# Performance work log

Hardware: AMD Instinct MI355X
Metric: run time of the kernel (lower is better)

## Reference

```python
import jax, jax.numpy as jnp
import numpy as np

FFT_LEN = 512
HOP_LEN = 256
N_BLOCK = 4
N_BIN = FFT_LEN // 2 + 1  # 257
STATE_FACTOR = 0.99999
ALPHA_E = 0.7
BETA_F = 0.1
BATCH = 4096
N_MIC = 1


def setup_inputs() -> dict:
    key = jax.random.key(0)
    ks = jax.random.split(key, 7)
    return {
        "mic": jax.random.normal(ks[0], (BATCH, HOP_LEN, N_MIC), jnp.float32),
        "loudspeaker_buffer": jax.random.normal(ks[1], (BATCH, (N_BLOCK + 1) * HOP_LEN), jnp.float32),
        "phi_e": jax.random.uniform(ks[2], (BATCH, N_BIN, N_MIC), jnp.float32),
        "phi_f": jax.random.uniform(ks[3], (BATCH, N_BIN, N_BLOCK, N_MIC), jnp.float32),
        "P1": jax.random.uniform(ks[4], (BATCH, N_BIN, N_BLOCK, N_MIC), jnp.float32),
        "H_post_real": 0.1 * jax.random.normal(ks[5], (BATCH, N_BIN, N_BLOCK, N_MIC), jnp.float32),
        "H_post_imag": 0.1 * jax.random.normal(ks[6], (BATCH, N_BIN, N_BLOCK, N_MIC), jnp.float32),
    }


def reference(mic, loudspeaker_buffer, phi_e, phi_f, P1, H_post_real, H_post_imag):
    B = mic.shape[0]
    sf2 = STATE_FACTOR * STATE_FACTOR
    H_post = jax.lax.complex(H_post_real, H_post_imag)  # [B, n_bin, n_block, n_mic]

    # STFT of loudspeaker buffer: rectangular window, center=False -> n_block frames
    frame_idx = jnp.arange(N_BLOCK)[:, None] * HOP_LEN + jnp.arange(FFT_LEN)[None, :]
    frames = loudspeaker_buffer[:, frame_idx]              # [B, n_block, fft_len]
    X = jnp.swapaxes(jnp.fft.rfft(frames, axis=-1), 1, 2)  # [B, n_bin, n_block]

    # zero-padded rFFT of mic frame
    zpad = jnp.zeros((B, FFT_LEN - HOP_LEN, N_MIC), mic.dtype)
    fd_mic = jnp.fft.rfft(jnp.concatenate([zpad, mic], axis=1), n=FFT_LEN, axis=1)  # [B, n_bin, n_mic]

    H_prior = H_post
    # a-priori feedback estimate
    fd_fb_hat = jnp.sum(X[..., None] * H_prior, axis=2)                     # [B, n_bin, n_mic]
    est_fb = jnp.fft.irfft(fd_fb_hat, FFT_LEN, axis=1)[:, HOP_LEN:, :]      # [B, hop, n_mic]
    fd_est_fb = jnp.fft.rfft(jnp.concatenate([zpad, est_fb], axis=1), n=FFT_LEN, axis=1)
    E = fd_mic - fd_est_fb                                                  # [B, n_bin, n_mic]

    phi_e = ALPHA_E * phi_e + (1.0 - ALPHA_E) * jnp.abs(E) ** 2

    # Kalman gain
    phi_f = BETA_F * phi_f + (1.0 - BETA_F) * jnp.abs(H_prior) ** 2
    phi_n = (1.0 - sf2) * phi_f
    Xr = jnp.abs(X) ** 2                                                    # [B, n_bin, n_block]
    U = Xr[..., None] * P1                                                  # [B, n_bin, n_block, n_mic]
    R = U + 2.0 * phi_e[:, :, None, :] + 1e-10
    K = P1 * jnp.conj(X)[..., None] / R                                     # [B, n_bin, n_block, n_mic]
    P0 = jax.lax.stop_gradient(P1) - 0.5 * jax.lax.stop_gradient(jnp.abs(K) ** 2 * R)
    P1_new = sf2 * P0 + phi_n  # state update (not part of returned output)

    # filter update via gradient-constrained overlap-save
    dH = jnp.fft.irfft(K * E[:, :, None, :], FFT_LEN, axis=1)               # [B, fft_len, n_block, n_mic]
    mask = (jnp.arange(FFT_LEN) < HOP_LEN).astype(dH.dtype)[None, :, None, None]
    fd_dH = jnp.fft.rfft(dH * mask, n=FFT_LEN, axis=1)                      # [B, n_bin, n_block, n_mic]
    H_post_new = STATE_FACTOR * (H_prior + fd_dH)

    # a-posteriori feedback estimate and enhanced frame
    fd_fb_hat2 = jnp.sum(X[..., None] * H_post_new, axis=2)
    est_fb2 = jnp.fft.irfft(fd_fb_hat2, FFT_LEN, axis=1)[:, HOP_LEN:, :]
    enhanced = mic - est_fb2                                                # [B, hop, n_mic]
    return enhanced
```

## Files before the change

### kernel.cpp

```cpp
#include <hip/hip_runtime.h>
#include <math.h>

#define SF 0.99999f
#define PI2 6.283185307179586476925f
#define SWZ(c) ((c) ^ (((c) >> 4) & 15))
#define LDSFENCE() asm volatile("" ::: "memory")

template<int SGN>
__device__ __forceinline__ void twmul(float& ur, float& ui, float c, float s) {
    const float ss = (SGN < 0) ? -s : s;
    const float r = ur * c - ui * ss;
    const float i = ui * c + ur * ss;
    ur = r; ui = i;
}

template<int SGN>
__device__ __forceinline__ void bfly8(float* ur, float* ui) {
    const float C2 = 0.70710678118654752440f;
    float ar[4], ai[4], br[4], bi[4];
#pragma unroll
    for (int m = 0; m < 4; ++m) {
        ar[m] = ur[m] + ur[m + 4]; ai[m] = ui[m] + ui[m + 4];
        br[m] = ur[m] - ur[m + 4]; bi[m] = ui[m] - ui[m + 4];
    }
    float b1r, b1i, b2r, b2i, b3r, b3i;
    if (SGN < 0) {
        b1r = C2 * (br[1] + bi[1]); b1i = C2 * (bi[1] - br[1]);
        b2r = bi[2];                b2i = -br[2];
        b3r = C2 * (bi[3] - br[3]); b3i = -C2 * (br[3] + bi[3]);
    } else {
        b1r = C2 * (br[1] - bi[1]); b1i = C2 * (bi[1] + br[1]);
        b2r = -bi[2];               b2i = br[2];
        b3r = -C2 * (br[3] + bi[3]); b3i = C2 * (br[3] - bi[3]);
    }
    const float e0r = ar[0] + ar[2], e0i = ai[0] + ai[2];
    const float e1r = ar[0] - ar[2], e1i = ai[0] - ai[2];
    const float o0r = ar[1] + ar[3], o0i = ai[1] + ai[3];
    const float o1r = ar[1] - ar[3], o1i = ai[1] - ai[3];
    ur[0] = e0r + o0r; ui[0] = e0i + o0i;
    ur[4] = e0r - o0r; ui[4] = e0i - o0i;
    if (SGN < 0) { ur[2] = e1r + o1i; ui[2] = e1i - o1r; ur[6] = e1r - o1i; ui[6] = e1i + o1r; }
    else         { ur[2] = e1r - o1i; ui[2] = e1i + o1r; ur[6] = e1r + o1i; ui[6] = e1i - o1r; }
    const float f0r = br[0] + b2r, f0i = bi[0] + b2i;
    const float f1r = br[0] - b2r, f1i = bi[0] - b2i;
    const float g0r = b1r + b3r, g0i = b1i + b3i;
    const float g1r = b1r - b3r, g1i = b1i - b3i;
    ur[1] = f0r + g0r; ui[1] = f0i + g0i;
    ur[5] = f0r - g0r; ui[5] = f0i - g0i;
    if (SGN < 0) { ur[3] = f1r + g1i; ui[3] = f1i - g1r; ur[7] = f1r - g1i; ui[7] = f1i + g1r; }
    else         { ur[3] = f1r - g1i; ui[3] = f1i + g1r; ur[7] = f1r + g1i; ui[7] = f1i - g1r; }
}

template<int SGN>
__device__ __forceinline__ void fft512w(float* ur, float* ui,
                                        float2* __restrict__ buf,
                                        const float2* __restrict__ tw2,
                                        const float2* __restrict__ tw3,
                                        const int* ra, int t) {
    bfly8<SGN>(ur, ui);
    LDSFENCE();
#pragma unroll
    for (int m = 0; m < 8; ++m) buf[SWZ(8 * t + m)] = make_float2(ur[m], ui[m]);
    LDSFENCE();
#pragma unroll
    for (int m = 0; m < 8; ++m) { const float2 v = buf[ra[m]]; ur[m] = v.x; ui[m] = v.y; }
    const int k2 = t & 7;
#pragma unroll
    for (int m = 1; m < 8; ++m) { const float2 w = tw2[m * 8 + k2]; twmul<SGN>(ur[m], ui[m], w.x, w.y); }
    bfly8<SGN>(ur, ui);
    const int jj = ((t >> 3) << 6) + k2;
    LDSFENCE();
#pragma unroll
    for (int m = 0; m < 8; ++m) buf[SWZ(jj + 8 * m)] = make_float2(ur[m], ui[m]);
    LDSFENCE();
#pragma unroll
    for (int m = 0; m < 8; ++m) { const float2 v = buf[ra[m]]; ur[m] = v.x; ui[m] = v.y; }
#pragma unroll
    for (int m = 1; m < 8; ++m) { const float2 w = tw3[m * 64 + t]; twmul<SGN>(ur[m], ui[m], w.x, w.y); }
    bfly8<SGN>(ur, ui);
    LDSFENCE();
}

__global__ __launch_bounds__(256, 2) void pbfd_kernel(
    const float* __restrict__ g_mic,
    const float* __restrict__ g_lsb,
    const float* __restrict__ g_phie,
    const float* __restrict__ g_p1,
    const float* __restrict__ g_hr,
    const float* __restrict__ g_hi,
    float* __restrict__ g_out,
    int B) {
    __shared__ float2 tw2[64];
    __shared__ float2 tw3[512];
    __shared__ float2 xch[4][512];

    const int tid = threadIdx.x;
    for (int e = tid; e < 512; e += 256) {
        const int m = e >> 6, tt = e & 63;
        float s, c;
        sincosf(PI2 * (float)(m * tt) * (1.0f / 512.0f), &s, &c);
        tw3[e] = make_float2(c, s);
    }
    if (tid < 64) {
        const int m = tid >> 3, k = tid & 7;
        float s, c;
        sincosf(PI2 * (float)(m * k) * (1.0f / 64.0f), &s, &c);
        tw2[tid] = make_float2(c, s);
    }
    __syncthreads();

    const int w = tid >> 6;
    const int t = tid & 63;
    const int elem = blockIdx.x * 4 + w;
    if (elem >= B) return;
    float2* buf = &xch[w][0];
    const int ml = (64 - t) & 63;

    int ra[8];
#pragma unroll
    for (int m = 0; m < 8; ++m) ra[m] = SWZ(t + 64 * m);

    float mv[4];
    {
        const float* mp = g_mic + (size_t)elem * 256;
#pragma unroll
        for (int q = 0; q < 4; ++q) mv[q] = mp[t + 64 * q];
    }

    float xr[4][4], xi[4][4], xn[4];
    {
        const float* lb = g_lsb + (size_t)elem * 1280;
#pragma unroll
        for (int pr = 0; pr < 2; ++pr) {
            float ur[8], ui[8];
#pragma unroll
            for (int m = 0; m < 8; ++m) {
                ur[m] = lb[(2 * pr) * 256 + t + 64 * m];
                ui[m] = lb[(2 * pr + 1) * 256 + t + 64 * m];
            }
            fft512w<-1>(ur, ui, buf, tw2, tw3, ra, t);
#pragma unroll
            for (int m = 0; m < 4; ++m) {
                float zmr = __shfl(ur[7 - m], ml);
                float zmi = __shfl(ui[7 - m], ml);
                if (t == 0) {
                    zmr = (m == 0) ? ur[0] : ur[8 - m];
                    zmi = (m == 0) ? ui[0] : ui[8 - m];
                }
                xr[2 * pr][m]     = 0.5f * (ur[m] + zmr);
                xi[2 * pr][m]     = 0.5f * (ui[m] - zmi);
                xr[2 * pr + 1][m] = 0.5f * (ui[m] + zmi);
                xi[2 * pr + 1][m] = -0.5f * (ur[m] - zmr);
            }
            if (t == 0) { xn[2 * pr] = ur[4]; xn[2 * pr + 1] = ui[4]; }
        }
    }

    auto herm_ifft = [&](const float cr[4], const float ci[4], float cn, float o4[4]) {
        float ur[8], ui[8];
#pragma unroll
        for (int m = 0; m < 4; ++m) { ur[m] = cr[m]; ui[m] = ci[m]; }
#pragma unroll
        for (int m = 4; m < 8; ++m) {
            ur[m] = __shfl(cr[7 - m], ml);
            ui[m] = -__shfl(ci[7 - m], ml);
        }
        if (t == 0) {
            ur[5] = cr[3]; ui[5] = -ci[3];
            ur[6] = cr[2]; ui[6] = -ci[2];
            ur[7] = cr[1]; ui[7] = -ci[1];
            ur[4] = cn; ui[4] = 0.f;
        }
        fft512w<1>(ur, ui, buf, tw2, tw3, ra, t);
#pragma unroll
        for (int q = 0; q < 4; ++q) o4[q] = ur[4 + q] * (1.0f / 512.0f);
    };

    float d4[4];
    float pn[4], en = 0.f, pen = 0.f;
    {
        float hr_[4][4], hi_[4][4], hn[4];
        {
            const float4* hr4 = (const float4*)g_hr + (size_t)elem * 257;
            const float4* hi4 = (const float4*)g_hi + (size_t)elem * 257;
#pragma unroll
            for (int m = 0; m < 4; ++m) {
                const float4 a = hr4[t + 64 * m];
                hr_[0][m] = a.x; hr_[1][m] = a.y; hr_[2][m] = a.z; hr_[3][m] = a.w;
            }
#pragma unroll
            for (int m = 0; m < 4; ++m) {
                const float4 b = hi4[t + 64 * m];
                hi_[0][m] = b.x; hi_[1][m] = b.y; hi_[2][m] = b.z; hi_[3][m] = b.w;
            }
            if (t == 0) {
                const float4 a = hr4[256];
                const float4 p = ((const float4*)g_p1)[(size_t)elem * 257 + 256];
                hn[0] = a.x; hn[1] = a.y; hn[2] = a.z; hn[3] = a.w;
                pn[0] = p.x; pn[1] = p.y; pn[2] = p.z; pn[3] = p.w;
            }
        }
        float cr[4], ci[4], cn = 0.f;
#pragma unroll
        for (int m = 0; m < 4; ++m) {
            float sr = 0.f, si = 0.f;
#pragma unroll
            for (int j = 0; j < 4; ++j) {
                sr += xr[j][m] * hr_[j][m] - xi[j][m] * hi_[j][m];
                si += xr[j][m] * hi_[j][m] + xi[j][m] * hr_[j][m];
            }
            cr[m] = sr; ci[m] = si;
        }
        if (t == 0) {
#pragma unroll
            for (int j = 0; j < 4; ++j) cn += xn[j] * hn[j];
        }
        float o4[4];
        herm_ifft(cr, ci, cn, o4);
#pragma unroll
        for (int q = 0; q < 4; ++q) d4[q] = mv[q] - o4[q];
    }

    float er[4], ei[4];
    {
        float ur[8], ui[8];
#pragma unroll
        for (int m = 0; m < 4; ++m) { ur[m] = 0.f; ui[m] = 0.f; }
#pragma unroll
        for (int q = 0; q < 4; ++q) { ur[4 + q] = d4[q]; ui[4 + q] = 0.f; }
        fft512w<-1>(ur, ui, buf, tw2, tw3, ra, t);
#pragma unroll
        for (int m = 0; m < 4; ++m) { er[m] = ur[m]; ei[m] = ui[m]; }
        if (t == 0) en = ur[4];
    }

    float pe[4];
    {
        const float* php = g_phie + (size_t)elem * 257;
#pragma unroll
        for (int m = 0; m < 4; ++m)
            pe[m] = 0.7f * php[t + 64 * m] + 0.3f * (er[m] * er[m] + ei[m] * ei[m]);
        if (t == 0) pen = 0.7f * php[256] + 0.3f * en * en;
    }

    float Dr[4] = {0, 0, 0, 0}, Di[4] = {0, 0, 0, 0};
    float dn = 0.f;
    {
        const float4* p14 = (const float4*)g_p1 + (size_t)elem * 257;
#pragma unroll
        for (int pr = 0; pr < 2; ++pr) {
            const int j0 = 2 * pr, j1 = 2 * pr + 1;
            float ur[8], ui[8], gr[4], gi[4];
#pragma unroll
            for (int m = 0; m < 4; ++m) {
                const float4 p = p14[t + 64 * m];
                const float pa = pr ? p.z : p.x;
                const float pb = pr ? p.w : p.y;
                const float xxa = xr[j0][m] * xr[j0][m] + xi[j0][m] * xi[j0][m];
                const float Ra = xxa * pa + 2.f * pe[m] + 1e-10f;
                const float ia = 1.f / Ra;
                const float kra = pa * xr[j0][m] * ia, kia = -pa * xi[j0][m] * ia;
                const float a_r = kra * er[m] - kia * ei[m];
                const float a_i = kra * ei[m] + kia * er[m];
                const float xxb = xr[j1][m] * xr[j1][m] + xi[j1][m] * xi[j1][m];
                const float Rb = xxb * pb + 2.f * pe[m] + 1e-10f;
                const float ib = 1.f / Rb;
                const float krb = pb * xr[j1][m] * ib, kib = -pb * xi[j1][m] * ib;
                const float b_r = krb * er[m] - kib * ei[m];
                const float b_i = krb * ei[m] + kib * er[m];
                ur[m] = a_r - b_i;  ui[m] = a_i + b_r;
                gr[m] = a_r + b_i;  gi[m] = b_r - a_i;
            }
#pragma unroll
            for (int m = 4; m < 8; ++m) {
                ur[m] = __shfl(gr[7 - m], ml);
                ui[m] = __shfl(gi[7 - m], ml);
            }
            if (t == 0) {
                ur[5] = gr[3]; ui[5] = gi[3];
                ur[6] = gr[2]; ui[6] = gi[2];
                ur[7] = gr[1]; ui[7] = gi[1];
                const float Rn0 = xn[j0] * xn[j0] * pn[j0] + 2.f * pen + 1e-10f;
                const float Rn1 = xn[j1] * xn[j1] * pn[j1] + 2.f * pen + 1e-10f;
                ur[4] = pn[j0] * xn[j0] / Rn0 * en;
                ui[4] = pn[j1] * xn[j1] / Rn1 * en;
            }
            fft512w<1>(ur, ui, buf, tw2, tw3, ra, t);
#pragma unroll
            for (int m = 0; m < 4; ++m) { ur[m] *= (1.0f / 512.0f); ui[m] *= (1.0f / 512.0f); }
#pragma unroll
            for (int m = 4; m < 8; ++m) { ur[m] = 0.f; ui[m] = 0.f; }
            fft512w<-1>(ur, ui, buf, tw2, tw3, ra, t);
#pragma unroll
            for (int m = 0; m < 4; ++m) {
                float zmr = __shfl(ur[7 - m], ml);
                float zmi = __shfl(ui[7 - m], ml);
                if (t == 0) {
                    zmr = (m == 0) ? ur[0] : ur[8 - m];
                    zmi = (m == 0) ? ui[0] : ui[8 - m];
                }
                const float f0r = 0.5f * (ur[m] + zmr), f0i = 0.5f * (ui[m] - zmi);
                const float f1r = 0.5f * (ui[m] + zmi), f1i = -0.5f * (ur[m] - zmr);
                Dr[m] += xr[j0][m] * f0r - xi[j0][m] * f0i + xr[j1][m] * f1r - xi[j1][m] * f1i;
                Di[m] += xr[j0][m] * f0i + xi[j0][m] * f0r + xr[j1][m] * f1i + xi[j1][m] * f1r;
            }
            if (t == 0) dn += xn[j0] * ur[4] + xn[j1] * ui[4];
        }
    }

    {
        float o4[4];
        herm_ifft(Dr, Di, dn, o4);
        float* op = g_out + (size_t)elem * 256;
#pragma unroll
        for (int q = 0; q < 4; ++q)
            op[t + 64 * q] = mv[q] - SF * ((mv[q] - d4[q]) + o4[q]);
    }
}

extern "C" void kernel_launch(void* const* d_in, const int* in_sizes, int n_in,
                              void* d_out, int out_size, void* d_ws, size_t ws_size,
                              hipStream_t stream) {
    const float* mic  = (const float*)d_in[0];
    const float* lsb  = (const float*)d_in[1];
    const float* phie = (const float*)d_in[2];
    const float* p1   = (const float*)d_in[4];
    const float* hr   = (const float*)d_in[5];
    const float* hi   = (const float*)d_in[6];
    float* out = (float*)d_out;

    const int B = in_sizes[0] / 256;
    const int blocks = (B + 3) / 4;
    pbfd_kernel<<<blocks, 256, 0, stream>>>(mic, lsb, phie, p1, hr, hi, out, B);
}
```

Measured before the change: 36.76 us.

## Launch one 64-thread wavefront per batch element with per-wave twiddle setup

Changes the launch from 256-thread blocks holding four batch elements to single-wavefront blocks that each handle one element. The block-wide __syncthreads after twiddle setup goes away, leaving only a compiler memory fence. Each wave now builds its own twiddle tables, and the 512-entry table is generated by repeated complex multiplication from one sincos instead of one sincos per entry. This cuts per-block LDS and removes cross-wave synchronization, but it multiplies twiddle setup work per element. Recurrence rounding may also slightly change twiddle accuracy.

```diff
diff --git a/kernel.cpp b/kernel.cpp
--- a/kernel.cpp
+++ b/kernel.cpp
@@ -81,40 +81,40 @@
     LDSFENCE();
 }
 
-__global__ __launch_bounds__(256, 2) void pbfd_kernel(
+__global__ __launch_bounds__(64, 4) void pbfd_kernel(
     const float* __restrict__ g_mic,
     const float* __restrict__ g_lsb,
     const float* __restrict__ g_phie,
     const float* __restrict__ g_p1,
     const float* __restrict__ g_hr,
     const float* __restrict__ g_hi,
-    float* __restrict__ g_out,
-    int B) {
+    float* __restrict__ g_out)
+{
     __shared__ float2 tw2[64];
     __shared__ float2 tw3[512];
-    __shared__ float2 xch[4][512];
-
-    const int tid = threadIdx.x;
-    for (int e = tid; e < 512; e += 256) {
-        const int m = e >> 6, tt = e & 63;
-        float s, c;
-        sincosf(PI2 * (float)(m * tt) * (1.0f / 512.0f), &s, &c);
-        tw3[e] = make_float2(c, s);
-    }
-    if (tid < 64) {
-        const int m = tid >> 3, k = tid & 7;
-        float s, c;
-        sincosf(PI2 * (float)(m * k) * (1.0f / 64.0f), &s, &c);
-        tw2[tid] = make_float2(c, s);
-    }
-    __syncthreads();
-
-    const int w = tid >> 6;
-    const int t = tid & 63;
-    const int elem = blockIdx.x * 4 + w;
-    if (elem >= B) return;
-    float2* buf = &xch[w][0];
+    __shared__ float2 xch[512];
+
+    const int t = threadIdx.x;
+    const int elem = blockIdx.x;
+    float2* buf = &xch[0];
     const int ml = (64 - t) & 63;
+
+    {
+        float s3, c3;
+        sincosf(PI2 * (float)t * (1.0f / 512.0f), &s3, &c3);
+        float cr = 1.f, ci = 0.f;
+#pragma unroll
+        for (int m = 0; m < 8; ++m) {
+            tw3[m * 64 + t] = make_float2(cr, ci);
+            const float nr = cr * c3 - ci * s3;
+            ci = ci * c3 + cr * s3;
+            cr = nr;
+        }
+        float s2, c2;
+        sincosf(PI2 * (float)((t >> 3) * (t & 7)) * (1.0f / 64.0f), &s2, &c2);
+        tw2[t] = make_float2(c2, s2);
+    }
+    LDSFENCE();
 
     int ra[8];
 #pragma unroll
@@ -330,6 +330,5 @@
     float* out = (float*)d_out;
 
     const int B = in_sizes[0] / 256;
-    const int blocks = (B + 3) / 4;
-    pbfd_kernel<<<blocks, 256, 0, stream>>>(mic, lsb, phie, p1, hr, hi, out, B);
-}
+    pbfd_kernel<<<B, 64, 0, stream>>>(mic, lsb, phie, p1, hr, hi, out);
+}
```

Result: slower. 50.19 us (+36.5%).

## Split each batch element across two wavefronts, one per block pair

Applied to the files above, without the earlier changes.

Each batch element now gets a 128-thread block, and each of its two wavefronts handles one pair of blocks (FFT of two frames, the filter product and the Kalman gradient). Partial sums for the feedback estimate and the filter update are combined through shared memory with block barriers, and only wave 0 runs the final inverse FFT and store. This halves per-wave serial work and register pressure, giving more parallelism. The cost is extra LDS traffic and syncs, the same work done twice (mic load, error FFT, phi_e), and wave 1 sitting idle at the end.

```diff
diff --git a/kernel.cpp b/kernel.cpp
--- a/kernel.cpp
+++ b/kernel.cpp
@@ -81,21 +81,28 @@
     LDSFENCE();
 }
 
-__global__ __launch_bounds__(256, 2) void pbfd_kernel(
+__global__ __launch_bounds__(128, 2) void pbfd_kernel(
     const float* __restrict__ g_mic,
     const float* __restrict__ g_lsb,
     const float* __restrict__ g_phie,
     const float* __restrict__ g_p1,
     const float* __restrict__ g_hr,
     const float* __restrict__ g_hi,
-    float* __restrict__ g_out,
-    int B) {
+    float* __restrict__ g_out)
+{
     __shared__ float2 tw2[64];
     __shared__ float2 tw3[512];
-    __shared__ float2 xch[4][512];
+    __shared__ float2 xch[2][512];
 
     const int tid = threadIdx.x;
-    for (int e = tid; e < 512; e += 256) {
+    const int w = tid >> 6;
+    const int t = tid & 63;
+    const int elem = blockIdx.x;
+    float2* buf  = &xch[w][0];
+    float2* bufo = &xch[1 ^ w][0];
+    const int ml = (64 - t) & 63;
+
+    for (int e = tid; e < 512; e += 128) {
         const int m = e >> 6, tt = e & 63;
         float s, c;
         sincosf(PI2 * (float)(m * tt) * (1.0f / 512.0f), &s, &c);
@@ -109,13 +116,6 @@
     }
     __syncthreads();
 
-    const int w = tid >> 6;
-    const int t = tid & 63;
-    const int elem = blockIdx.x * 4 + w;
-    if (elem >= B) return;
-    float2* buf = &xch[w][0];
-    const int ml = (64 - t) & 63;
-
     int ra[8];
 #pragma unroll
     for (int m = 0; m < 8; ++m) ra[m] = SWZ(t + 64 * m);
@@ -127,33 +127,30 @@
         for (int q = 0; q < 4; ++q) mv[q] = mp[t + 64 * q];
     }
 
-    float xr[4][4], xi[4][4], xn[4];
+    float xrl[2][4], xil[2][4], xnl[2];
     {
         const float* lb = g_lsb + (size_t)elem * 1280;
-#pragma unroll
-        for (int pr = 0; pr < 2; ++pr) {
-            float ur[8], ui[8];
-#pragma unroll
-            for (int m = 0; m < 8; ++m) {
-                ur[m] = lb[(2 * pr) * 256 + t + 64 * m];
-                ui[m] = lb[(2 * pr + 1) * 256 + t + 64 * m];
+        float ur[8], ui[8];
+#pragma unroll
+        for (int m = 0; m < 8; ++m) {
+            ur[m] = lb[(2 * w) * 256 + t + 64 * m];
+            ui[m] = lb[(2 * w + 1) * 256 + t + 64 * m];
+        }
+        fft512w<-1>(ur, ui, buf, tw2, tw3, ra, t);
+#pragma unroll
+        for (int m = 0; m < 4; ++m) {
+            float zmr = __shfl(ur[7 - m], ml);
+            float zmi = __shfl(ui[7 - m], ml);
+            if (t == 0) {
+                zmr = (m == 0) ? ur[0] : ur[8 - m];
+                zmi = (m == 0) ? ui[0] : ui[8 - m];
             }
-            fft512w<-1>(ur, ui, buf, tw2, tw3, ra, t);
-#pragma unroll
-            for (int m = 0; m < 4; ++m) {
-                float zmr = __shfl(ur[7 - m], ml);
-                float zmi = __shfl(ui[7 - m], ml);
-                if (t == 0) {
-                    zmr = (m == 0) ? ur[0] : ur[8 - m];
-                    zmi = (m == 0) ? ui[0] : ui[8 - m];
-                }
-                xr[2 * pr][m]     = 0.5f * (ur[m] + zmr);
-                xi[2 * pr][m]     = 0.5f * (ui[m] - zmi);
-                xr[2 * pr + 1][m] = 0.5f * (ui[m] + zmi);
-                xi[2 * pr + 1][m] = -0.5f * (ur[m] - zmr);
-            }
-            if (t == 0) { xn[2 * pr] = ur[4]; xn[2 * pr + 1] = ui[4]; }
-        }
+            xrl[0][m] = 0.5f * (ur[m] + zmr);
+            xil[0][m] = 0.5f * (ui[m] - zmi);
+            xrl[1][m] = 0.5f * (ui[m] + zmi);
+            xil[1][m] = -0.5f * (ur[m] - zmr);
+        }
+        if (t == 0) { xnl[0] = ur[4]; xnl[1] = ui[4]; }
     }
 
     auto herm_ifft = [&](const float cr[4], const float ci[4], float cn, float o4[4]) {
@@ -177,44 +174,38 @@
     };
 
     float d4[4];
-    float pn[4], en = 0.f, pen = 0.f;
-    {
-        float hr_[4][4], hi_[4][4], hn[4];
+    float pnl[2] = {0, 0}, en = 0.f, pen = 0.f;
+    {
+        float cr[4], ci[4], cn = 0.f;
         {
-            const float4* hr4 = (const float4*)g_hr + (size_t)elem * 257;
-            const float4* hi4 = (const float4*)g_hi + (size_t)elem * 257;
+            const float2* hr2 = (const float2*)(g_hr + (size_t)elem * 1028);
+            const float2* hi2 = (const float2*)(g_hi + (size_t)elem * 1028);
 #pragma unroll
             for (int m = 0; m < 4; ++m) {
-                const float4 a = hr4[t + 64 * m];
-                hr_[0][m] = a.x; hr_[1][m] = a.y; hr_[2][m] = a.z; hr_[3][m] = a.w;
-            }
-#pragma unroll
-            for (int m = 0; m < 4; ++m) {
-                const float4 b = hi4[t + 64 * m];
-                hi_[0][m] = b.x; hi_[1][m] = b.y; hi_[2][m] = b.z; hi_[3][m] = b.w;
+                const int bin = t + 64 * m;
+                const float2 a = hr2[bin * 2 + w];
+                const float2 b = hi2[bin * 2 + w];
+                cr[m] = xrl[0][m] * a.x - xil[0][m] * b.x + xrl[1][m] * a.y - xil[1][m] * b.y;
+                ci[m] = xrl[0][m] * b.x + xil[0][m] * a.x + xrl[1][m] * b.y + xil[1][m] * a.y;
             }
             if (t == 0) {
-                const float4 a = hr4[256];
-                const float4 p = ((const float4*)g_p1)[(size_t)elem * 257 + 256];
-                hn[0] = a.x; hn[1] = a.y; hn[2] = a.z; hn[3] = a.w;
-                pn[0] = p.x; pn[1] = p.y; pn[2] = p.z; pn[3] = p.w;
+                const float2 a = hr2[256 * 2 + w];
+                const float2 p = ((const float2*)(g_p1 + (size_t)elem * 1028))[256 * 2 + w];
+                cn = xnl[0] * a.x + xnl[1] * a.y;
+                pnl[0] = p.x; pnl[1] = p.y;
             }
         }
-        float cr[4], ci[4], cn = 0.f;
+#pragma unroll
+        for (int m = 0; m < 4; ++m) buf[t + 64 * m] = make_float2(cr[m], ci[m]);
+        if (t == 0) buf[256] = make_float2(cn, 0.f);
+        __syncthreads();
 #pragma unroll
         for (int m = 0; m < 4; ++m) {
-            float sr = 0.f, si = 0.f;
-#pragma unroll
-            for (int j = 0; j < 4; ++j) {
-                sr += xr[j][m] * hr_[j][m] - xi[j][m] * hi_[j][m];
-                si += xr[j][m] * hi_[j][m] + xi[j][m] * hr_[j][m];
-            }
-            cr[m] = sr; ci[m] = si;
-        }
-        if (t == 0) {
-#pragma unroll
-            for (int j = 0; j < 4; ++j) cn += xn[j] * hn[j];
-        }
+            const float2 v = bufo[t + 64 * m];
+            cr[m] += v.x; ci[m] += v.y;
+        }
+        if (t == 0) cn += bufo[256].x;
+        __syncthreads();
         float o4[4];
         herm_ifft(cr, ci, cn, o4);
 #pragma unroll
@@ -243,72 +234,79 @@
         if (t == 0) pen = 0.7f * php[256] + 0.3f * en * en;
     }
 
-    float Dr[4] = {0, 0, 0, 0}, Di[4] = {0, 0, 0, 0};
+    float Dr[4], Di[4];
     float dn = 0.f;
     {
-        const float4* p14 = (const float4*)g_p1 + (size_t)elem * 257;
-#pragma unroll
-        for (int pr = 0; pr < 2; ++pr) {
-            const int j0 = 2 * pr, j1 = 2 * pr + 1;
-            float ur[8], ui[8], gr[4], gi[4];
-#pragma unroll
-            for (int m = 0; m < 4; ++m) {
-                const float4 p = p14[t + 64 * m];
-                const float pa = pr ? p.z : p.x;
-                const float pb = pr ? p.w : p.y;
-                const float xxa = xr[j0][m] * xr[j0][m] + xi[j0][m] * xi[j0][m];
-                const float Ra = xxa * pa + 2.f * pe[m] + 1e-10f;
-                const float ia = 1.f / Ra;
-                const float kra = pa * xr[j0][m] * ia, kia = -pa * xi[j0][m] * ia;
-                const float a_r = kra * er[m] - kia * ei[m];
-                const float a_i = kra * ei[m] + kia * er[m];
-                const float xxb = xr[j1][m] * xr[j1][m] + xi[j1][m] * xi[j1][m];
-                const float Rb = xxb * pb + 2.f * pe[m] + 1e-10f;
-                const float ib = 1.f / Rb;
-                const float krb = pb * xr[j1][m] * ib, kib = -pb * xi[j1][m] * ib;
-                const float b_r = krb * er[m] - kib * ei[m];
-                const float b_i = krb * ei[m] + kib * er[m];
-                ur[m] = a_r - b_i;  ui[m] = a_i + b_r;
-                gr[m] = a_r + b_i;  gi[m] = b_r - a_i;
+        const float2* p12 = (const float2*)(g_p1 + (size_t)elem * 1028);
+        float ur[8], ui[8], gr[4], gi[4];
+#pragma unroll
+        for (int m = 0; m < 4; ++m) {
+            const float2 p = p12[(t + 64 * m) * 2 + w];
+            const float pa = p.x, pb = p.y;
+            const float xxa = xrl[0][m] * xrl[0][m] + xil[0][m] * xil[0][m];
+            const float Ra = xxa * pa + 2.f * pe[m] + 1e-10f;
+            const float ia = 1.f / Ra;
+            const float kra = pa * xrl[0][m] * ia, kia = -pa * xil[0][m] * ia;
+            const float a_r = kra * er[m] - kia * ei[m];
+            const float a_i = kra * ei[m] + kia * er[m];
+            const float xxb = xrl[1][m] * xrl[1][m] + xil[1][m] * xil[1][m];
+            const float Rb = xxb * pb + 2.f * pe[m] + 1e-10f;
+            const float ib = 1.f / Rb;
+            const float krb = pb * xrl[1][m] * ib, kib = -pb * xil[1][m] * ib;
+            const float b_r = krb * er[m] - kib * ei[m];
+            const float b_i = krb * ei[m] + kib * er[m];
+            ur[m] = a_r - b_i;  ui[m] = a_i + b_r;
+            gr[m] = a_r + b_i;  gi[m] = b_r - a_i;
+        }
+#pragma unroll
+        for (int m = 4; m < 8; ++m) {
+            ur[m] = __shfl(gr[7 - m], ml);
+            ui[m] = __shfl(gi[7 - m], ml);
+        }
+        if (t == 0) {
+            ur[5] = gr[3]; ui[5] = gi[3];
+            ur[6] = gr[2]; ui[6] = gi[2];
+            ur[7] = gr[1]; ui[7] = gi[1];
+            const float Rn0 = xnl[0] * xnl[0] * pnl[0] + 2.f * pen + 1e-10f;
+            const float Rn1 = xnl[1] * xnl[1] * pnl[1] + 2.f * pen + 1e-10f;
+            ur[4] = pnl[0] * xnl[0] / Rn0 * en;
+            ui[4] = pnl[1] * xnl[1] / Rn1 * en;
+        }
+        fft512w<1>(ur, ui, buf, tw2, tw3, ra, t);
+#pragma unroll
+        for (int m = 0; m < 4; ++m) { ur[m] *= (1.0f / 512.0f); ui[m] *= (1.0f / 512.0f); }
+#pragma unroll
+        for (int m = 4; m < 8; ++m) { ur[m] = 0.f; ui[m] = 0.f; }
+        fft512w<-1>(ur, ui, buf, tw2, tw3, ra, t);
+#pragma unroll
+        for (int m = 0; m < 4; ++m) {
+            float zmr = __shfl(ur[7 - m], ml);
+            float zmi = __shfl(ui[7 - m], ml);
+            if (t == 0) {
+                zmr = (m == 0) ? ur[0] : ur[8 - m];
+                zmi = (m == 0) ? ui[0] : ui[8 - m];
             }
-#pragma unroll
-            for (int m = 4; m < 8; ++m) {
-                ur[m] = __shfl(gr[7 - m], ml);
-                ui[m] = __shfl(gi[7 - m], ml);
-            }
-            if (t == 0) {
-                ur[5] = gr[3]; ui[5] = gi[3];
-                ur[6] = gr[2]; ui[6] = gi[2];
-                ur[7] = gr[1]; ui[7] = gi[1];
-                const float Rn0 = xn[j0] * xn[j0] * pn[j0] + 2.f * pen + 1e-10f;
-                const float Rn1 = xn[j1] * xn[j1] * pn[j1] + 2.f * pen + 1e-10f;
-                ur[4] = pn[j0] * xn[j0] / Rn0 * en;
-                ui[4] = pn[j1] * xn[j1] / Rn1 * en;
-            }
-            fft512w<1>(ur, ui, buf, tw2, tw3, ra, t);
-#pragma unroll
-            for (int m = 0; m < 4; ++m) { ur[m] *= (1.0f / 512.0f); ui[m] *= (1.0f / 512.0f); }
-#pragma unroll
-            for (int m = 4; m < 8; ++m) { ur[m] = 0.f; ui[m] = 0.f; }
-            fft512w<-1>(ur, ui, buf, tw2, tw3, ra, t);
-#pragma unroll
-            for (int m = 0; m < 4; ++m) {
-                float zmr = __shfl(ur[7 - m], ml);
-                float zmi = __shfl(ui[7 - m], ml);
-                if (t == 0) {
-                    zmr = (m == 0) ? ur[0] : ur[8 - m];
-                    zmi = (m == 0) ? ui[0] : ui[8 - m];
-                }
-                const float f0r = 0.5f * (ur[m] + zmr), f0i = 0.5f * (ui[m] - zmi);
-                const float f1r = 0.5f * (ui[m] + zmi), f1i = -0.5f * (ur[m] - zmr);
-                Dr[m] += xr[j0][m] * f0r - xi[j0][m] * f0i + xr[j1][m] * f1r - xi[j1][m] * f1i;
-                Di[m] += xr[j0][m] * f0i + xi[j0][m] * f0r + xr[j1][m] * f1i + xi[j1][m] * f1r;
-            }
-            if (t == 0) dn += xn[j0] * ur[4] + xn[j1] * ui[4];
-        }
-    }
-
-    {
+            const float f0r = 0.5f * (ur[m] + zmr), f0i = 0.5f * (ui[m] - zmi);
+            const float f1r = 0.5f * (ui[m] + zmi), f1i = -0.5f * (ur[m] - zmr);
+            Dr[m] = xrl[0][m] * f0r - xil[0][m] * f0i + xrl[1][m] * f1r - xil[1][m] * f1i;
+            Di[m] = xrl[0][m] * f0i + xil[0][m] * f0r + xrl[1][m] * f1i + xil[1][m] * f1r;
+        }
+        if (t == 0) dn = xnl[0] * ur[4] + xnl[1] * ui[4];
+    }
+
+#pragma unroll
+    for (int m = 0; m < 4; ++m) buf[t + 64 * m] = make_float2(Dr[m], Di[m]);
+    if (t == 0) buf[256] = make_float2(dn, 0.f);
+    __syncthreads();
+#pragma unroll
+    for (int m = 0; m < 4; ++m) {
+        const float2 v = bufo[t + 64 * m];
+        Dr[m] += v.x; Di[m] += v.y;
+    }
+    if (t == 0) dn += bufo[256].x;
+    __syncthreads();
+
+    if (w == 0) {
         float o4[4];
         herm_ifft(Dr, Di, dn, o4);
         float* op = g_out + (size_t)elem * 256;
@@ -330,6 +328,5 @@
     float* out = (float*)d_out;
 
     const int B = in_sizes[0] / 256;
-    const int blocks = (B + 3) / 4;
-    pbfd_kernel<<<blocks, 256, 0, stream>>>(mic, lsb, phie, p1, hr, hi, out, B);
-}
+    pbfd_kernel<<<B, 128, 0, stream>>>(mic, lsb, phie, p1, hr, hi, out);
+}
```

New measurement: 41.80 us. 1.14x slower.
